# Performance work log

Measured on AMD Instinct MI355X. Metric: run time of the kernel, lower is better.

The kernel has to match this reference:

```python
import jax, jax.numpy as jnp
import numpy as np

EMBED_DIM = 512
NUM_HEADS = 8
HEAD_DIM = EMBED_DIM // NUM_HEADS
LN_EPS = 1e-5


def setup_inputs() -> dict:
    key = jax.random.key(0)
    ks = jax.random.split(key, 7)
    B, S, E = 2, 4096, EMBED_DIM
    s = 1.0 / np.sqrt(E)
    return {
        "x": jax.random.normal(ks[0], (B, S, E), dtype=jnp.float32),
        "qkv_w": jax.random.normal(ks[1], (E, 3 * E), dtype=jnp.float32) * s,
        "qkv_b": jax.random.normal(ks[2], (3 * E,), dtype=jnp.float32) * 0.01,
        "out_w": jax.random.normal(ks[3], (E, E), dtype=jnp.float32) * s,
        "out_b": jax.random.normal(ks[4], (E,), dtype=jnp.float32) * 0.01,
        "ln_g": jnp.ones((E,), dtype=jnp.float32),
        "ln_b": jnp.zeros((E,), dtype=jnp.float32),
    }


def reference(x, qkv_w, qkv_b, out_w, out_b, ln_g, ln_b):
    B, S, E = x.shape
    H, D = NUM_HEADS, HEAD_DIM
    scale = D ** -0.5
    qkv = x @ qkv_w + qkv_b                     # (B, S, 3E)
    qkv = qkv.reshape(B, S, 3, H, D)
    q, k, v = qkv[:, :, 0], qkv[:, :, 1], qkv[:, :, 2]  # (B, S, H, D)
    scores = jnp.einsum("bshd,bthd->bhst", q, k) * scale  # (B, H, S, S)
    probs = jax.nn.softmax(scores, axis=-1)
    ctx = jnp.einsum("bhst,bthd->bshd", probs, v).reshape(B, S, E)
    out = ctx @ out_w + out_b + x               # residual
    mu = out.mean(-1, keepdims=True)
    var = out.var(-1, keepdims=True)
    return (out - mu) * jax.lax.rsqrt(var + LN_EPS) * ln_g + ln_b
```

## Files before the change

kernel.cpp:

```cpp
#include <hip/hip_runtime.h>
#include <stdint.h>

typedef __bf16 bf16x8 __attribute__((ext_vector_type(8)));
typedef float f32x4 __attribute__((ext_vector_type(4)));
typedef float f32x16 __attribute__((ext_vector_type(16)));
typedef float float4v __attribute__((ext_vector_type(4)));
typedef unsigned short u16x4 __attribute__((ext_vector_type(4)));
typedef unsigned short u16x8 __attribute__((ext_vector_type(8)));
typedef unsigned int u32x4v __attribute__((ext_vector_type(4)));

#define DEVI __device__ __forceinline__

static constexpr int Bv = 2, Sv = 4096, Ev = 512, Hv = 8, Dv = 64;
static constexpr int Mv = Bv * Sv;
static constexpr int N3v = 3 * Ev;
static constexpr float QSCALE = 0.125f * 1.4426950408889634f;
static constexpr float C0 = -8.0f;

#if __has_builtin(__builtin_amdgcn_exp2f)
#define EXP2F(x) __builtin_amdgcn_exp2f(x)
#else
#define EXP2F(x) exp2f(x)
#endif

DEVI unsigned short f2bf(float f) {
    unsigned int u = __builtin_bit_cast(unsigned int, f);
    u += 0x7fffu + ((u >> 16) & 1u);
    return (unsigned short)(u >> 16);
}

DEVI float b2f(unsigned short u) {
    return __builtin_bit_cast(float, (unsigned int)u << 16);
}

DEVI unsigned int cvtpk(float lo, float hi) {
    unsigned int r;
    asm("v_cvt_pk_bf16_f32 %0, %1, %2" : "=v"(r) : "v"(lo), "v"(hi));
    return r;
}

DEVI void gload16(const void* src, void* lds) {
    __builtin_amdgcn_global_load_lds(
        (const __attribute__((address_space(1))) unsigned int*)src,
        (__attribute__((address_space(3))) unsigned int*)lds,
        16, 0, 0);
}

__global__ __launch_bounds__(256) void k_convert(const float* __restrict__ in,
                                                 unsigned short* __restrict__ out, int n4) {
    int i = blockIdx.x * 256 + threadIdx.x;
    int stride = gridDim.x * 256;
    for (; i < n4; i += stride) {
        float4v v = ((const float4v*)in)[i];
        u16x4 o;
        o[0] = f2bf(v[0]); o[1] = f2bf(v[1]); o[2] = f2bf(v[2]); o[3] = f2bf(v[3]);
        ((u16x4*)out)[i] = o;
    }
}

__global__ __launch_bounds__(256) void k_tconv(const float* __restrict__ in,
                                               unsigned short* __restrict__ out, int K, int N) {
    __shared__ float lds[32][36];
    int tilesN = N >> 5;
    int tn = blockIdx.x % tilesN, tk = blockIdx.x / tilesN;
    int k0 = tk << 5, n0 = tn << 5;
    int t = threadIdx.x;
    int r = t >> 3, c4 = (t & 7) << 2;
    float4v v = *(const float4v*)(in + (size_t)(k0 + r) * N + n0 + c4);
    *(float4v*)&lds[r][c4] = v;
    __syncthreads();
    int nn = t >> 3, kc = (t & 7) << 2;
    u16x4 o;
#pragma unroll
    for (int j = 0; j < 4; ++j) o[j] = f2bf(lds[kc + j][nn]);
    *(u16x4*)(out + (size_t)(n0 + nn) * K + k0 + kc) = o;
}

template <int EPI>
__global__ __launch_bounds__(256) void k_gemm(
    const unsigned short* __restrict__ A, const unsigned short* __restrict__ Bt,
    int M, int N, int K, const float* __restrict__ bias,
    unsigned short* __restrict__ Qb, unsigned short* __restrict__ Kb,
    unsigned short* __restrict__ Vtb,
    const float* __restrict__ xres, float* __restrict__ outf) {
    __shared__ char smem[32768];
    char* As = smem;
    char* Bs = smem + 16384;
    int nbt = N >> 7;
    int mb = blockIdx.x / nbt, nbi = blockIdx.x % nbt;
    int m0 = mb << 7, n0 = nbi << 7;
    int tid = threadIdx.x, lane = tid & 63, wave = tid >> 6;
    int wr = wave >> 1, wc = wave & 1;

    f32x4 acc[4][4];
    f32x4 zero = {0.f, 0.f, 0.f, 0.f};
#pragma unroll
    for (int a = 0; a < 4; ++a)
#pragma unroll
        for (int b = 0; b < 4; ++b) acc[a][b] = zero;

    for (int kt = 0; kt < K; kt += 64) {
        __syncthreads();
#pragma unroll
        for (int j = 0; j < 4; ++j) {
            int la = (((wave << 2) + j) << 10) + lane * 16;
            int r = la >> 7, cb = la & 127;
            int cbs = cb ^ ((r & 7) << 4);
            gload16((const char*)(A + (size_t)(m0 + r) * K + kt) + cbs,
                    As + (((wave << 2) + j) << 10));
            gload16((const char*)(Bt + (size_t)(n0 + r) * K + kt) + cbs,
                    Bs + (((wave << 2) + j) << 10));
        }
        asm volatile("s_waitcnt vmcnt(0)" ::: "memory");
        __syncthreads();

        bf16x8 af[4][2], bfr[4][2];
#pragma unroll
        for (int rf = 0; rf < 4; ++rf)
#pragma unroll
            for (int c = 0; c < 2; ++c) {
                int row = (wr << 6) + (rf << 4) + (lane & 15);
                int col = (c << 6) + ((lane >> 4) << 4);
                af[rf][c] = *(const bf16x8*)(As + row * 128 + (col ^ ((row & 7) << 4)));
                int rowb = (wc << 6) + (rf << 4) + (lane & 15);
                bfr[rf][c] = *(const bf16x8*)(Bs + rowb * 128 + (col ^ ((rowb & 7) << 4)));
            }
#pragma unroll
        for (int rf = 0; rf < 4; ++rf)
#pragma unroll
            for (int nf = 0; nf < 4; ++nf)
#pragma unroll
                for (int c = 0; c < 2; ++c)
                    acc[rf][nf] = __builtin_amdgcn_mfma_f32_16x16x32_bf16(
                        af[rf][c], bfr[nf][c], acc[rf][nf], 0, 0, 0);
    }

#pragma unroll
    for (int rf = 0; rf < 4; ++rf)
#pragma unroll
        for (int nf = 0; nf < 4; ++nf) {
            int row0 = m0 + (wr << 6) + (rf << 4) + ((lane >> 4) << 2);
            int col = n0 + (wc << 6) + (nf << 4) + (lane & 15);
            float bv = bias[col];
            if (EPI == 0) {
                int reg = col >> 9, hd = col & 511;
                int h = hd >> 6, d = hd & 63;
                int b = row0 >> 12, s0 = row0 & 4095;
                if (reg == 2) {
                    u16x4 o4;
#pragma unroll
                    for (int i = 0; i < 4; ++i) o4[i] = f2bf(acc[rf][nf][i] + bv);
                    *(u16x4*)(Vtb + ((size_t)((b << 3) + h) * 64 + d) * 4096 + s0) = o4;
                } else {
#pragma unroll
                    for (int i = 0; i < 4; ++i) {
                        float v = acc[rf][nf][i] + bv;
                        size_t idx = ((size_t)((b << 3) + h) * Sv + s0 + i) * Dv + d;
                        if (reg == 0) Qb[idx] = f2bf(v * QSCALE);
                        else          Kb[idx] = f2bf(v);
                    }
                }
            } else {
#pragma unroll
                for (int i = 0; i < 4; ++i) {
                    int row = row0 + i;
                    float v = acc[rf][nf][i] + bv + xres[(size_t)row * N + col];
                    outf[(size_t)row * N + col] = v;
                }
            }
        }
}

__global__ __launch_bounds__(256, 2) void k_attn(const unsigned short* __restrict__ Qb,
                                                 const unsigned short* __restrict__ Kb,
                                                 const unsigned short* __restrict__ Vtb,
                                                 unsigned short* __restrict__ po,
                                                 float* __restrict__ pl) {
    __shared__ char smem[24576];
    int bid = blockIdx.x;
    int wg = ((bid & 7) << 7) + (bid >> 3);
    int quarter = wg & 3, qblk = (wg >> 2) & 15, bh = wg >> 6;
    int tid = threadIdx.x, lane = tid & 63, wave = tid >> 6;
    int l31 = lane & 31, hh = lane >> 5;
    int qbase = (qblk << 8) + (wave << 6);
    int kvbase = quarter << 10;
    const int NCH = 32;

    const char* Kbase = (const char*)(Kb + (size_t)bh * Sv * Dv + (size_t)kvbase * Dv);
    const char* Vtbase = (const char*)(Vtb + (size_t)bh * Dv * Sv + kvbase);

    bf16x8 qf[2][4];
#pragma unroll
    for (int qs = 0; qs < 2; ++qs)
#pragma unroll
        for (int tp = 0; tp < 4; ++tp)
            qf[qs][tp] = *(const bf16x8*)(Qb + ((size_t)bh * Sv + qbase + (qs << 5) + l31) * Dv +
                                          (tp << 4) + (hh << 3));

    const char* src0;
    const char* src1;
    size_t st0, st1;
    int d0, d1;
    {
        int j0 = wave << 1, j1 = j0 + 1;
        if (j0 < 4) {
            int lo0 = (j0 << 10) + lane * 16, r0 = lo0 >> 7, cb0 = lo0 & 127;
            src0 = Kbase + (size_t)r0 * 128 + (cb0 ^ ((r0 & 7) << 4));
            st0 = 4096; d0 = j0 << 10;
            int lo1 = (j1 << 10) + lane * 16, r1 = lo1 >> 7, cb1 = lo1 & 127;
            src1 = Kbase + (size_t)r1 * 128 + (cb1 ^ ((r1 & 7) << 4));
            st1 = 4096; d1 = j1 << 10;
        } else {
            int lo0 = ((j0 - 4) << 10) + lane * 16, r0 = lo0 >> 6, cb0 = lo0 & 63;
            src0 = Vtbase + (size_t)r0 * 8192 + (cb0 ^ ((r0 & 6) << 3));
            st0 = 64; d0 = 4096 + ((j0 - 4) << 10);
            int lo1 = ((j1 - 4) << 10) + lane * 16, r1 = lo1 >> 6, cb1 = lo1 & 63;
            src1 = Vtbase + (size_t)r1 * 8192 + (cb1 ^ ((r1 & 6) << 3));
            st1 = 64; d1 = 4096 + ((j1 - 4) << 10);
        }
    }

    int koff[4], voff[4];
#pragma unroll
    for (int tp = 0; tp < 4; ++tp)
        koff[tp] = l31 * 128 + (((tp << 5) + (hh << 4)) ^ ((l31 & 7) << 4));
#pragma unroll
    for (int tl = 0; tl < 2; ++tl)
#pragma unroll
        for (int dt = 0; dt < 2; ++dt) {
            int row = (dt << 5) + l31;
            int col = (tl << 5) + (hh << 4);
            voff[tl * 2 + dt] = row * 64 + (col ^ ((row & 6) << 3));
        }

    f32x16 o[2][2];
#pragma unroll
    for (int qs = 0; qs < 2; ++qs)
#pragma unroll
        for (int dt = 0; dt < 2; ++dt)
#pragma unroll
            for (int r = 0; r < 16; ++r) o[qs][dt][r] = 0.f;
    float lsum[2] = {0.f, 0.f};

    gload16(src0, smem + d0);
    gload16(src1, smem + d1);
    gload16(src0 + st0, smem + 8192 + d0);
    gload16(src1 + st1, smem + 8192 + d1);

#define COMPUTE_CHUNK(KSP, VSP)                                                          \
    {                                                                                    \
        bf16x8 kf[4], vf[4];                                                             \
        _Pragma("unroll") for (int tp = 0; tp < 4; ++tp)                                 \
            kf[tp] = *(const bf16x8*)((KSP) + koff[tp]);                                 \
        _Pragma("unroll") for (int i = 0; i < 4; ++i)                                    \
            vf[i] = *(const bf16x8*)((VSP) + voff[i]);                                   \
        _Pragma("unroll") for (int qs = 0; qs < 2; ++qs) {                               \
            f32x16 sc;                                                                   \
            _Pragma("unroll") for (int r = 0; r < 16; ++r) sc[r] = C0;                   \
            __builtin_amdgcn_s_setprio(1);                                               \
            _Pragma("unroll") for (int tp = 0; tp < 4; ++tp)                             \
                sc = __builtin_amdgcn_mfma_f32_32x32x16_bf16(kf[tp], qf[qs][tp], sc, 0, 0, 0); \
            __builtin_amdgcn_s_setprio(0);                                               \
            _Pragma("unroll") for (int r = 0; r < 16; ++r) sc[r] = EXP2F(sc[r]);         \
            float s0 = (sc[0] + sc[1]) + (sc[2] + sc[3]);                                \
            float s1 = (sc[4] + sc[5]) + (sc[6] + sc[7]);                                \
            float s2 = (sc[8] + sc[9]) + (sc[10] + sc[11]);                              \
            float s3 = (sc[12] + sc[13]) + (sc[14] + sc[15]);                            \
            lsum[qs] += (s0 + s1) + (s2 + s3);                                           \
            unsigned int W[8];                                                           \
            _Pragma("unroll") for (int i = 0; i < 8; ++i)                                \
                W[i] = cvtpk(sc[2 * i], sc[2 * i + 1]);                                  \
            _Pragma("unroll") for (int tl = 0; tl < 2; ++tl) {                           \
                unsigned int a1 = W[4 * tl], b1 = W[4 * tl + 2];                         \
                unsigned int a2 = W[4 * tl + 1], b2 = W[4 * tl + 3];                     \
                asm volatile("v_permlane32_swap_b32 %0, %1" : "+v"(a1), "+v"(b1));       \
                asm volatile("v_permlane32_swap_b32 %0, %1" : "+v"(a2), "+v"(b2));       \
                u32x4v uu;                                                               \
                uu[0] = a1; uu[1] = a2; uu[2] = b1; uu[3] = b2;                          \
                bf16x8 pf = __builtin_bit_cast(bf16x8, uu);                              \
                __builtin_amdgcn_s_setprio(1);                                           \
                _Pragma("unroll") for (int dt = 0; dt < 2; ++dt)                         \
                    o[qs][dt] = __builtin_amdgcn_mfma_f32_32x32x16_bf16(                 \
                        vf[tl * 2 + dt], pf, o[qs][dt], 0, 0, 0);                        \
                __builtin_amdgcn_s_setprio(0);                                           \
            }                                                                            \
        }                                                                                \
    }

    int cur = 0;
    for (int kt = 0; kt < NCH - 1; ++kt) {
        asm volatile("s_waitcnt vmcnt(2)\n\ts_barrier" ::: "memory");
        if (kt + 2 < NCH) {
            int tb = cur + 2; if (tb >= 3) tb -= 3;
            gload16(src0 + (size_t)(kt + 2) * st0, smem + tb * 8192 + d0);
            gload16(src1 + (size_t)(kt + 2) * st1, smem + tb * 8192 + d1);
        }
        char* cbuf = smem + cur * 8192;
        COMPUTE_CHUNK(cbuf, cbuf + 4096);
        cur = (cur + 1 == 3) ? 0 : cur + 1;
    }
    asm volatile("s_waitcnt vmcnt(0)\n\ts_barrier" ::: "memory");
    {
        char* cbuf = smem + cur * 8192;
        COMPUTE_CHUNK(cbuf, cbuf + 4096);
    }
#undef COMPUTE_CHUNK

#pragma unroll
    for (int qs = 0; qs < 2; ++qs) {
        float ls = lsum[qs] + __shfl_xor(lsum[qs], 32, 64);
        int qrow = qbase + (qs << 5) + l31;
        if (!hh) pl[((size_t)quarter * 16 + bh) * Sv + qrow] = ls;
        size_t obase = (((size_t)quarter * 16 + bh) * Sv + qrow) * 64;
#pragma unroll
        for (int dt = 0; dt < 2; ++dt)
#pragma unroll
            for (int rp = 0; rp < 8; ++rp) {
                int r = rp << 1;
                int d = (dt << 5) + (r & 3) + ((r >> 2) << 3) + (hh << 2);
                unsigned int w = cvtpk(o[qs][dt][r], o[qs][dt][r + 1]);
                *(unsigned int*)(po + obase + d) = w;
            }
    }
}

__global__ __launch_bounds__(256) void k_merge(const unsigned short* __restrict__ po,
                                               const float* __restrict__ pl,
                                               unsigned short* __restrict__ ctx) {
    int t = blockIdx.x * 256 + threadIdx.x;
    int d8 = t & 7, s = (t >> 3) & 4095, bh = t >> 15;
    int b = bh >> 3, h = bh & 7;
    size_t base = ((size_t)bh * 4096 + s) * 64 + (d8 << 3);
    const size_t Q = (size_t)16 * 4096 * 64;
    float a[8] = {0.f, 0.f, 0.f, 0.f, 0.f, 0.f, 0.f, 0.f};
    float l = 0.f;
#pragma unroll
    for (int q = 0; q < 4; ++q) {
        u16x8 p = *(const u16x8*)(po + q * Q + base);
#pragma unroll
        for (int j = 0; j < 8; ++j) a[j] += b2f(p[j]);
        l += pl[((size_t)q * 16 + bh) * 4096 + s];
    }
    float inv = 1.f / l;
    u32x4v w;
#pragma unroll
    for (int j = 0; j < 4; ++j) w[j] = cvtpk(a[2 * j] * inv, a[2 * j + 1] * inv);
    *(u32x4v*)(ctx + ((size_t)b * 4096 + s) * 512 + (h << 6) + (d8 << 3)) = w;
}

__global__ __launch_bounds__(256) void k_ln(const float* __restrict__ in,
                                            const float* __restrict__ g,
                                            const float* __restrict__ bta,
                                            float* __restrict__ out) {
    int wave = threadIdx.x >> 6, lane = threadIdx.x & 63;
    size_t row = (size_t)blockIdx.x * 4 + wave;
    const float* p = in + row * 512 + lane * 8;
    float4v v0 = *(const float4v*)p;
    float4v v1 = *(const float4v*)(p + 4);
    float s = 0.f, q = 0.f;
#pragma unroll
    for (int j = 0; j < 4; ++j) {
        s += v0[j] + v1[j];
        q += v0[j] * v0[j] + v1[j] * v1[j];
    }
#pragma unroll
    for (int off = 1; off < 64; off <<= 1) {
        s += __shfl_xor(s, off, 64);
        q += __shfl_xor(q, off, 64);
    }
    float mu = s * (1.f / 512.f);
    float var = q * (1.f / 512.f) - mu * mu;
    float rs = rsqrtf(var + 1e-5f);
    int c = lane * 8;
    float4v o0, o1;
#pragma unroll
    for (int j = 0; j < 4; ++j) {
        o0[j] = (v0[j] - mu) * rs * g[c + j] + bta[c + j];
        o1[j] = (v1[j] - mu) * rs * g[c + 4 + j] + bta[c + 4 + j];
    }
    *(float4v*)(out + row * 512 + c) = o0;
    *(float4v*)(out + row * 512 + c + 4) = o1;
}

extern "C" void kernel_launch(void* const* d_in, const int* in_sizes, int n_in,
                              void* d_out, int out_size, void* d_ws, size_t ws_size,
                              hipStream_t stream) {
    const float* x     = (const float*)d_in[0];
    const float* qkv_w = (const float*)d_in[1];
    const float* qkv_b = (const float*)d_in[2];
    const float* out_w = (const float*)d_in[3];
    const float* out_b = (const float*)d_in[4];
    const float* ln_g  = (const float*)d_in[5];
    const float* ln_b  = (const float*)d_in[6];
    float* out = (float*)d_out;
    char* ws = (char*)d_ws;

    unsigned short* owT   = (unsigned short*)(ws);
    unsigned short* wqkvT = (unsigned short*)(ws + 524288);
    unsigned short* Qb    = (unsigned short*)(ws + 2097152);
    unsigned short* Kb    = (unsigned short*)(ws + 10485760);
    unsigned short* Vtb   = (unsigned short*)(ws + 18874368);
    unsigned short* xb    = (unsigned short*)(ws + 27262976);
    unsigned short* po    = (unsigned short*)(ws + 27262976);
    float* pl             = (float*)(ws + 60817408);
    unsigned short* ctxb  = (unsigned short*)(ws + 2097152);
    float* tmp            = (float*)(ws + 27262976);

    k_convert<<<2048, 256, 0, stream>>>(x, xb, Mv * Ev / 4);
    k_tconv<<<(512 / 32) * (1536 / 32), 256, 0, stream>>>(qkv_w, wqkvT, 512, 1536);
    k_tconv<<<(512 / 32) * (512 / 32), 256, 0, stream>>>(out_w, owT, 512, 512);
    k_gemm<0><<<(Mv / 128) * (N3v / 128), 256, 0, stream>>>(
        xb, wqkvT, Mv, N3v, Ev, qkv_b, Qb, Kb, Vtb, nullptr, nullptr);
    k_attn<<<1024, 256, 0, stream>>>(Qb, Kb, Vtb, po, pl);
    k_merge<<<2048, 256, 0, stream>>>(po, pl, ctxb);
    k_gemm<1><<<(Mv / 128) * (Ev / 128), 256, 0, stream>>>(
        ctxb, owT, Mv, Ev, Ev, out_b, nullptr, nullptr, nullptr, x, tmp);
    k_ln<<<Mv / 4, 256, 0, stream>>>(tmp, ln_g, ln_b, out);
}
```

Before: 156.2 us.

## Software-pipeline attention loop so PV MFMAs overlap next chunk's exp and pack

```diff
diff --git a/kernel.cpp b/kernel.cpp
--- a/kernel.cpp
+++ b/kernel.cpp
@@ -242,18 +242,19 @@
             for (int r = 0; r < 16; ++r) o[qs][dt][r] = 0.f;
     float lsum[2] = {0.f, 0.f};
 
+    bf16x8 vfp[4];
+    bf16x8 pfp[2][2];
+
     gload16(src0, smem + d0);
     gload16(src1, smem + d1);
     gload16(src0 + st0, smem + 8192 + d0);
     gload16(src1 + st1, smem + 8192 + d1);
 
-#define COMPUTE_CHUNK(KSP, VSP)                                                          \
+#define QK_PACK(KSP)                                                                     \
     {                                                                                    \
-        bf16x8 kf[4], vf[4];                                                             \
+        bf16x8 kf[4];                                                                    \
         _Pragma("unroll") for (int tp = 0; tp < 4; ++tp)                                 \
             kf[tp] = *(const bf16x8*)((KSP) + koff[tp]);                                 \
-        _Pragma("unroll") for (int i = 0; i < 4; ++i)                                    \
-            vf[i] = *(const bf16x8*)((VSP) + voff[i]);                                   \
         _Pragma("unroll") for (int qs = 0; qs < 2; ++qs) {                               \
             f32x16 sc;                                                                   \
             _Pragma("unroll") for (int r = 0; r < 16; ++r) sc[r] = C0;                   \
@@ -277,34 +278,142 @@
                 asm volatile("v_permlane32_swap_b32 %0, %1" : "+v"(a2), "+v"(b2));       \
                 u32x4v uu;                                                               \
                 uu[0] = a1; uu[1] = a2; uu[2] = b1; uu[3] = b2;                          \
-                bf16x8 pf = __builtin_bit_cast(bf16x8, uu);                              \
-                __builtin_amdgcn_s_setprio(1);                                           \
+                pfp[qs][tl] = __builtin_bit_cast(bf16x8, uu);                            \
+            }                                                                            \
+        }                                                                                \
+    }
+
+#define PV_PREV()                                                                        \
+    {                                                                                    \
+        __builtin_amdgcn_s_setprio(1);                                                   \
+        _Pragma("unroll") for (int qs = 0; qs < 2; ++qs)                                 \
+            _Pragma("unroll") for (int tl = 0; tl < 2; ++tl)                             \
                 _Pragma("unroll") for (int dt = 0; dt < 2; ++dt)                         \
                     o[qs][dt] = __builtin_amdgcn_mfma_f32_32x32x16_bf16(                 \
-                        vf[tl * 2 + dt], pf, o[qs][dt], 0, 0, 0);                        \
-                __builtin_amdgcn_s_setprio(0);                                           \
-            }                                                                            \
-        }                                                                                \
-    }
-
-    int cur = 0;
-    for (int kt = 0; kt < NCH - 1; ++kt) {
-        asm volatile("s_waitcnt vmcnt(2)\n\ts_barrier" ::: "memory");
-        if (kt + 2 < NCH) {
-            int tb = cur + 2; if (tb >= 3) tb -= 3;
-            gload16(src0 + (size_t)(kt + 2) * st0, smem + tb * 8192 + d0);
-            gload16(src1 + (size_t)(kt + 2) * st1, smem + tb * 8192 + d1);
+                        vfp[tl * 2 + dt], pfp[qs][tl], o[qs][dt], 0, 0, 0);              \
+        __builtin_amdgcn_s_setprio(0);                                                   \
+    }
+
+#define LOAD_VF(VSP)                                                                     \
+    _Pragma("unroll") for (int i = 0; i < 4; ++i)                                        \
+        vfp[i] = *(const bf16x8*)((VSP) + voff[i]);
+
+    asm volatile("s_waitcnt vmcnt(2)\n\ts_barrier" ::: "memory");
+    gload16(src0 + 2 * st0, smem + 16384 + d0);
+    gload16(src1 + 2 * st1, smem + 16384 + d1);
+    QK_PACK(smem);
+    LOAD_VF(smem + 4096);
+
+    for (int kt = 1; kt < NCH - 1; ++kt) {
+        asm volatile("s_waitcnt lgkmcnt(0)\n\ts_waitcnt vmcnt(2)\n\ts_barrier" ::: "memory");
+        int tb = (kt + 2) % 3;
+        gload16(src0 + (size_t)(kt + 2) * st0, smem + tb * 8192 + d0);
+        gload16(src1 + (size_t)(kt + 2) * st1, smem + tb * 8192 + d1);
+        char* cbuf = smem + (kt % 3) * 8192;
+        bf16x8 kf[4];
+#pragma unroll
+        for (int tp = 0; tp < 4; ++tp) kf[tp] = *(const bf16x8*)(cbuf + koff[tp]);
+        f32x16 sc0, sc1;
+#pragma unroll
+        for (int r = 0; r < 16; ++r) { sc0[r] = C0; sc1[r] = C0; }
+        __builtin_amdgcn_s_setprio(1);
+#pragma unroll
+        for (int tp = 0; tp < 4; ++tp)
+            sc0 = __builtin_amdgcn_mfma_f32_32x32x16_bf16(kf[tp], qf[0][tp], sc0, 0, 0, 0);
+#pragma unroll
+        for (int tp = 0; tp < 4; ++tp)
+            sc1 = __builtin_amdgcn_mfma_f32_32x32x16_bf16(kf[tp], qf[1][tp], sc1, 0, 0, 0);
+#pragma unroll
+        for (int qs = 0; qs < 2; ++qs)
+#pragma unroll
+            for (int tl = 0; tl < 2; ++tl)
+#pragma unroll
+                for (int dt = 0; dt < 2; ++dt)
+                    o[qs][dt] = __builtin_amdgcn_mfma_f32_32x32x16_bf16(
+                        vfp[tl * 2 + dt], pfp[qs][tl], o[qs][dt], 0, 0, 0);
+        __builtin_amdgcn_s_setprio(0);
+#pragma unroll
+        for (int qs = 0; qs < 2; ++qs) {
+            f32x16 sc = qs ? sc1 : sc0;
+#pragma unroll
+            for (int r = 0; r < 16; ++r) sc[r] = EXP2F(sc[r]);
+            float s0 = (sc[0] + sc[1]) + (sc[2] + sc[3]);
+            float s1 = (sc[4] + sc[5]) + (sc[6] + sc[7]);
+            float s2 = (sc[8] + sc[9]) + (sc[10] + sc[11]);
+            float s3 = (sc[12] + sc[13]) + (sc[14] + sc[15]);
+            lsum[qs] += (s0 + s1) + (s2 + s3);
+            unsigned int W[8];
+#pragma unroll
+            for (int i = 0; i < 8; ++i) W[i] = cvtpk(sc[2 * i], sc[2 * i + 1]);
+#pragma unroll
+            for (int tl = 0; tl < 2; ++tl) {
+                unsigned int a1 = W[4 * tl], b1 = W[4 * tl + 2];
+                unsigned int a2 = W[4 * tl + 1], b2 = W[4 * tl + 3];
+                asm volatile("v_permlane32_swap_b32 %0, %1" : "+v"(a1), "+v"(b1));
+                asm volatile("v_permlane32_swap_b32 %0, %1" : "+v"(a2), "+v"(b2));
+                u32x4v uu;
+                uu[0] = a1; uu[1] = a2; uu[2] = b1; uu[3] = b2;
+                pfp[qs][tl] = __builtin_bit_cast(bf16x8, uu);
+            }
         }
-        char* cbuf = smem + cur * 8192;
-        COMPUTE_CHUNK(cbuf, cbuf + 4096);
-        cur = (cur + 1 == 3) ? 0 : cur + 1;
-    }
-    asm volatile("s_waitcnt vmcnt(0)\n\ts_barrier" ::: "memory");
+        LOAD_VF(cbuf + 4096);
+    }
+
+    asm volatile("s_waitcnt lgkmcnt(0)\n\ts_waitcnt vmcnt(0)\n\ts_barrier" ::: "memory");
     {
-        char* cbuf = smem + cur * 8192;
-        COMPUTE_CHUNK(cbuf, cbuf + 4096);
-    }
-#undef COMPUTE_CHUNK
+        char* cbuf = smem + ((NCH - 1) % 3) * 8192;
+        bf16x8 kf[4];
+#pragma unroll
+        for (int tp = 0; tp < 4; ++tp) kf[tp] = *(const bf16x8*)(cbuf + koff[tp]);
+        f32x16 sc0, sc1;
+#pragma unroll
+        for (int r = 0; r < 16; ++r) { sc0[r] = C0; sc1[r] = C0; }
+        __builtin_amdgcn_s_setprio(1);
+#pragma unroll
+        for (int tp = 0; tp < 4; ++tp)
+            sc0 = __builtin_amdgcn_mfma_f32_32x32x16_bf16(kf[tp], qf[0][tp], sc0, 0, 0, 0);
+#pragma unroll
+        for (int tp = 0; tp < 4; ++tp)
+            sc1 = __builtin_amdgcn_mfma_f32_32x32x16_bf16(kf[tp], qf[1][tp], sc1, 0, 0, 0);
+#pragma unroll
+        for (int qs = 0; qs < 2; ++qs)
+#pragma unroll
+            for (int tl = 0; tl < 2; ++tl)
+#pragma unroll
+                for (int dt = 0; dt < 2; ++dt)
+                    o[qs][dt] = __builtin_amdgcn_mfma_f32_32x32x16_bf16(
+                        vfp[tl * 2 + dt], pfp[qs][tl], o[qs][dt], 0, 0, 0);
+        __builtin_amdgcn_s_setprio(0);
+#pragma unroll
+        for (int qs = 0; qs < 2; ++qs) {
+            f32x16 sc = qs ? sc1 : sc0;
+#pragma unroll
+            for (int r = 0; r < 16; ++r) sc[r] = EXP2F(sc[r]);
+            float s0 = (sc[0] + sc[1]) + (sc[2] + sc[3]);
+            float s1 = (sc[4] + sc[5]) + (sc[6] + sc[7]);
+            float s2 = (sc[8] + sc[9]) + (sc[10] + sc[11]);
+            float s3 = (sc[12] + sc[13]) + (sc[14] + sc[15]);
+            lsum[qs] += (s0 + s1) + (s2 + s3);
+            unsigned int W[8];
+#pragma unroll
+            for (int i = 0; i < 8; ++i) W[i] = cvtpk(sc[2 * i], sc[2 * i + 1]);
+#pragma unroll
+            for (int tl = 0; tl < 2; ++tl) {
+                unsigned int a1 = W[4 * tl], b1 = W[4 * tl + 2];
+                unsigned int a2 = W[4 * tl + 1], b2 = W[4 * tl + 3];
+                asm volatile("v_permlane32_swap_b32 %0, %1" : "+v"(a1), "+v"(b1));
+                asm volatile("v_permlane32_swap_b32 %0, %1" : "+v"(a2), "+v"(b2));
+                u32x4v uu;
+                uu[0] = a1; uu[1] = a2; uu[2] = b1; uu[3] = b2;
+                pfp[qs][tl] = __builtin_bit_cast(bf16x8, uu);
+            }
+        }
+        LOAD_VF(cbuf + 4096);
+        PV_PREV();
+    }
+#undef QK_PACK
+#undef PV_PREV
+#undef LOAD_VF
 
 #pragma unroll
     for (int qs = 0; qs < 2; ++qs) {
```

New measurement: 159.7 us. 2.2% more time.

## Stagger attention waves so odd waves defer PV MFMAs to overlap exp with MFMA

Applied to the files above, without the earlier changes.

```diff
diff --git a/kernel.cpp b/kernel.cpp
--- a/kernel.cpp
+++ b/kernel.cpp
@@ -185,6 +185,7 @@
     int qbase = (qblk << 8) + (wave << 6);
     int kvbase = quarter << 10;
     const int NCH = 32;
+    int par = (wave ^ (bid >> 3)) & 1;
 
     const char* Kbase = (const char*)(Kb + (size_t)bh * Sv * Dv + (size_t)kvbase * Dv);
     const char* Vtbase = (const char*)(Vtb + (size_t)bh * Dv * Sv + kvbase);
@@ -242,69 +243,101 @@
             for (int r = 0; r < 16; ++r) o[qs][dt][r] = 0.f;
     float lsum[2] = {0.f, 0.f};
 
+    bf16x8 vfp[4];
+    bf16x8 pfp[2][2];
+
     gload16(src0, smem + d0);
     gload16(src1, smem + d1);
     gload16(src0 + st0, smem + 8192 + d0);
     gload16(src1 + st1, smem + 8192 + d1);
 
-#define COMPUTE_CHUNK(KSP, VSP)                                                          \
+#define QK8(CB, SC0, SC1)                                                                \
     {                                                                                    \
-        bf16x8 kf[4], vf[4];                                                             \
+        bf16x8 kf[4];                                                                    \
         _Pragma("unroll") for (int tp = 0; tp < 4; ++tp)                                 \
-            kf[tp] = *(const bf16x8*)((KSP) + koff[tp]);                                 \
-        _Pragma("unroll") for (int i = 0; i < 4; ++i)                                    \
-            vf[i] = *(const bf16x8*)((VSP) + voff[i]);                                   \
-        _Pragma("unroll") for (int qs = 0; qs < 2; ++qs) {                               \
-            f32x16 sc;                                                                   \
-            _Pragma("unroll") for (int r = 0; r < 16; ++r) sc[r] = C0;                   \
-            __builtin_amdgcn_s_setprio(1);                                               \
-            _Pragma("unroll") for (int tp = 0; tp < 4; ++tp)                             \
-                sc = __builtin_amdgcn_mfma_f32_32x32x16_bf16(kf[tp], qf[qs][tp], sc, 0, 0, 0); \
-            __builtin_amdgcn_s_setprio(0);                                               \
-            _Pragma("unroll") for (int r = 0; r < 16; ++r) sc[r] = EXP2F(sc[r]);         \
-            float s0 = (sc[0] + sc[1]) + (sc[2] + sc[3]);                                \
-            float s1 = (sc[4] + sc[5]) + (sc[6] + sc[7]);                                \
-            float s2 = (sc[8] + sc[9]) + (sc[10] + sc[11]);                              \
-            float s3 = (sc[12] + sc[13]) + (sc[14] + sc[15]);                            \
-            lsum[qs] += (s0 + s1) + (s2 + s3);                                           \
-            unsigned int W[8];                                                           \
-            _Pragma("unroll") for (int i = 0; i < 8; ++i)                                \
-                W[i] = cvtpk(sc[2 * i], sc[2 * i + 1]);                                  \
-            _Pragma("unroll") for (int tl = 0; tl < 2; ++tl) {                           \
-                unsigned int a1 = W[4 * tl], b1 = W[4 * tl + 2];                         \
-                unsigned int a2 = W[4 * tl + 1], b2 = W[4 * tl + 3];                     \
-                asm volatile("v_permlane32_swap_b32 %0, %1" : "+v"(a1), "+v"(b1));       \
-                asm volatile("v_permlane32_swap_b32 %0, %1" : "+v"(a2), "+v"(b2));       \
-                u32x4v uu;                                                               \
-                uu[0] = a1; uu[1] = a2; uu[2] = b1; uu[3] = b2;                          \
-                bf16x8 pf = __builtin_bit_cast(bf16x8, uu);                              \
-                __builtin_amdgcn_s_setprio(1);                                           \
-                _Pragma("unroll") for (int dt = 0; dt < 2; ++dt)                         \
-                    o[qs][dt] = __builtin_amdgcn_mfma_f32_32x32x16_bf16(                 \
-                        vf[tl * 2 + dt], pf, o[qs][dt], 0, 0, 0);                        \
-                __builtin_amdgcn_s_setprio(0);                                           \
-            }                                                                            \
+            kf[tp] = *(const bf16x8*)((CB) + koff[tp]);                                  \
+        _Pragma("unroll") for (int r = 0; r < 16; ++r) { SC0[r] = C0; SC1[r] = C0; }     \
+        __builtin_amdgcn_s_setprio(1);                                                   \
+        _Pragma("unroll") for (int tp = 0; tp < 4; ++tp)                                 \
+            SC0 = __builtin_amdgcn_mfma_f32_32x32x16_bf16(kf[tp], qf[0][tp], SC0, 0, 0, 0); \
+        _Pragma("unroll") for (int tp = 0; tp < 4; ++tp)                                 \
+            SC1 = __builtin_amdgcn_mfma_f32_32x32x16_bf16(kf[tp], qf[1][tp], SC1, 0, 0, 0); \
+        __builtin_amdgcn_s_setprio(0);                                                   \
+    }
+
+#define EXPPACK(SCVAR, QS, PFARR)                                                        \
+    {                                                                                    \
+        _Pragma("unroll") for (int r = 0; r < 16; ++r) SCVAR[r] = EXP2F(SCVAR[r]);       \
+        float s0 = (SCVAR[0] + SCVAR[1]) + (SCVAR[2] + SCVAR[3]);                        \
+        float s1 = (SCVAR[4] + SCVAR[5]) + (SCVAR[6] + SCVAR[7]);                        \
+        float s2 = (SCVAR[8] + SCVAR[9]) + (SCVAR[10] + SCVAR[11]);                      \
+        float s3 = (SCVAR[12] + SCVAR[13]) + (SCVAR[14] + SCVAR[15]);                    \
+        lsum[QS] += (s0 + s1) + (s2 + s3);                                               \
+        unsigned int W[8];                                                               \
+        _Pragma("unroll") for (int i = 0; i < 8; ++i)                                    \
+            W[i] = cvtpk(SCVAR[2 * i], SCVAR[2 * i + 1]);                                \
+        _Pragma("unroll") for (int tl = 0; tl < 2; ++tl) {                               \
+            unsigned int a1 = W[4 * tl], b1 = W[4 * tl + 2];                             \
+            unsigned int a2 = W[4 * tl + 1], b2 = W[4 * tl + 3];                         \
+            asm volatile("v_permlane32_swap_b32 %0, %1" : "+v"(a1), "+v"(b1));           \
+            asm volatile("v_permlane32_swap_b32 %0, %1" : "+v"(a2), "+v"(b2));           \
+            u32x4v uu; uu[0] = a1; uu[1] = a2; uu[2] = b1; uu[3] = b2;                   \
+            PFARR[QS][tl] = __builtin_bit_cast(bf16x8, uu);                              \
         }                                                                                \
     }
 
-    int cur = 0;
-    for (int kt = 0; kt < NCH - 1; ++kt) {
-        asm volatile("s_waitcnt vmcnt(2)\n\ts_barrier" ::: "memory");
+#define PV8(VF, PF)                                                                      \
+    {                                                                                    \
+        __builtin_amdgcn_s_setprio(1);                                                   \
+        _Pragma("unroll") for (int q2 = 0; q2 < 2; ++q2)                                 \
+            _Pragma("unroll") for (int t2 = 0; t2 < 2; ++t2)                             \
+                _Pragma("unroll") for (int d2 = 0; d2 < 2; ++d2)                         \
+                    o[q2][d2] = __builtin_amdgcn_mfma_f32_32x32x16_bf16(                 \
+                        (VF)[t2 * 2 + d2], (PF)[q2][t2], o[q2][d2], 0, 0, 0);            \
+        __builtin_amdgcn_s_setprio(0);                                                   \
+    }
+
+#define RDVF(VB, VF)                                                                     \
+    _Pragma("unroll") for (int i = 0; i < 4; ++i)                                        \
+        (VF)[i] = *(const bf16x8*)((VB) + voff[i]);
+
+    for (int kt = 0; kt < NCH; ++kt) {
+        if (kt < NCH - 1)
+            asm volatile("s_waitcnt lgkmcnt(0)\n\ts_waitcnt vmcnt(2)\n\ts_barrier" ::: "memory");
+        else
+            asm volatile("s_waitcnt lgkmcnt(0)\n\ts_waitcnt vmcnt(0)\n\ts_barrier" ::: "memory");
         if (kt + 2 < NCH) {
-            int tb = cur + 2; if (tb >= 3) tb -= 3;
+            int tb = (kt + 2) % 3;
             gload16(src0 + (size_t)(kt + 2) * st0, smem + tb * 8192 + d0);
             gload16(src1 + (size_t)(kt + 2) * st1, smem + tb * 8192 + d1);
         }
-        char* cbuf = smem + cur * 8192;
-        COMPUTE_CHUNK(cbuf, cbuf + 4096);
-        cur = (cur + 1 == 3) ? 0 : cur + 1;
-    }
-    asm volatile("s_waitcnt vmcnt(0)\n\ts_barrier" ::: "memory");
-    {
-        char* cbuf = smem + cur * 8192;
-        COMPUTE_CHUNK(cbuf, cbuf + 4096);
-    }
-#undef COMPUTE_CHUNK
+        char* cbuf = smem + (kt % 3) * 8192;
+        char* vb = cbuf + 4096;
+
+        if (!par) {
+            bf16x8 vfl[4];
+            bf16x8 pfl[2][2];
+            RDVF(vb, vfl);
+            f32x16 sc0, sc1;
+            QK8(cbuf, sc0, sc1);
+            EXPPACK(sc0, 0, pfl);
+            EXPPACK(sc1, 1, pfl);
+            PV8(vfl, pfl);
+        } else {
+            if (kt > 0) PV8(vfp, pfp);
+            f32x16 sc0, sc1;
+            QK8(cbuf, sc0, sc1);
+            EXPPACK(sc0, 0, pfp);
+            EXPPACK(sc1, 1, pfp);
+            RDVF(vb, vfp);
+        }
+    }
+    if (par) PV8(vfp, pfp);
+
+#undef QK8
+#undef EXPPACK
+#undef PV8
+#undef RDVF
 
 #pragma unroll
     for (int qs = 0; qs < 2; ++qs) {
```

Measured after the change: 160.9 us. 1.03x slower.
